# Optimization experiments

Measured on AMD Instinct MI355X. Metric: run time of the kernel, lower is better.

Reference implementation:

```python
import jax, jax.numpy as jnp
import numpy as np

B, T, S, R, D, F = 256, 8, 200, 8, 64, 20


def setup_inputs() -> dict:
    key = jax.random.key(0)
    ks = jax.random.split(key, 8)
    # 0.1 scale keeps attention logits in a reasonable range (like trained embeddings)
    seq = 0.1 * jax.random.normal(ks[0], (B, S, D), dtype=jnp.float32)
    delta_t_n = jax.random.uniform(ks[1], (B, S), dtype=jnp.float32)  # normalized time gaps
    target = 0.1 * jax.random.normal(ks[2], (B, T, D), dtype=jnp.float32)
    target_value = 0.1 * jax.random.normal(ks[3], (B, T, R, D), dtype=jnp.float32)
    valid_mask = jax.random.randint(ks[4], (B, 1, S, 1), 0, 2, dtype=jnp.int32)
    rel_emb = 0.1 * jax.random.normal(ks[5], (R, D), dtype=jnp.float32)
    freq_real = 0.1 * jax.random.normal(ks[6], (R, F), dtype=jnp.float32)
    freq_imag = 0.1 * jax.random.normal(ks[7], (R, F), dtype=jnp.float32)
    return dict(seq=seq, delta_t_n=delta_t_n, target=target, target_value=target_value,
                valid_mask=valid_mask, rel_emb=rel_emb, freq_real=freq_real, freq_imag=freq_imag)


def _idft_decay(delta_t_n, freq_real, freq_imag):
    # freqs: concat(linspace(0,1,F)/2, -linspace(0,1,F)/2) -> [2F]
    f = jnp.linspace(0.0, 1.0, F, dtype=jnp.float32) / 2.0
    freqs = jnp.concatenate([f, -f])
    x_real = jnp.concatenate([freq_real, freq_real], axis=-1)   # [R,2F]
    x_imag = jnp.concatenate([freq_imag, -freq_imag], axis=-1)  # [R,2F]
    w = 2.0 * jnp.pi * freqs * delta_t_n[..., None]             # [B,S,2F]
    # [B,S,1,2F] * [1,1,R,2F] -> mean over 2F -> [B,S,R]
    decay = (jnp.cos(w)[:, :, None, :] * x_real[None, None]
             - jnp.sin(w)[:, :, None, :] * x_imag[None, None]).mean(axis=-1) / 2.0
    return decay


def reference(seq, delta_t_n, target, target_value, valid_mask, rel_emb, freq_real, freq_imag):
    # include_val=True branch
    rv = rel_emb[None, None] + target_value              # [B,T,R,D]
    ri = rv * target[:, :, None, :]                      # [B,T,R,D]
    # scores: contraction over D, no [B,T,S,R,D] materialization
    att = jnp.einsum('bsd,btrd->btsr', seq, ri)          # [B,T,S,R]
    att = att - att.max()
    att = jnp.where(valid_mask == 0, -jnp.inf, att)
    att = jax.nn.softmax(att, axis=-2)                   # softmax over seq (S)
    decay = jnp.clip(_idft_decay(delta_t_n, freq_real, freq_imag), 0.0, 1.0)[:, None]  # [B,1,S,R]
    decay = jnp.where(valid_mask == 0, 0.0, decay)
    att = att * decay
    context = jnp.einsum('bsd,btsr->btrd', seq, att)     # [B,T,R,D]
    return context
```

## Files before the change

kernel.cpp:

```cpp
#include <hip/hip_runtime.h>
#include <math.h>

constexpr int kB = 256, kT = 8, kS = 200, kR = 8, kD = 64, kF = 20;

constexpr float kW1 = 3.14159265358979323846f / 19.0f;

__global__ __launch_bounds__(256) void decay_kernel(
    const float* __restrict__ dt,
    const float* __restrict__ fr,
    const float* __restrict__ fi,
    const int*   __restrict__ vm,
    float* __restrict__ dec)
{
    const int b = blockIdx.x;
    const int tid = threadIdx.x;
    const int r = tid >> 5, j = tid & 31;

    float frr[kF], fir[kF];
    {
        const float4* f4 = (const float4*)(fr + r * kF);
        const float4* g4 = (const float4*)(fi + r * kF);
#pragma unroll
        for (int c = 0; c < 5; ++c) {
            float4 a = f4[c], g = g4[c];
            frr[4 * c + 0] = a.x; frr[4 * c + 1] = a.y;
            frr[4 * c + 2] = a.z; frr[4 * c + 3] = a.w;
            fir[4 * c + 0] = g.x; fir[4 * c + 1] = g.y;
            fir[4 * c + 2] = g.z; fir[4 * c + 3] = g.w;
        }
    }

#pragma unroll
    for (int it = 0; it < 7; ++it) {
        const int s = j + 32 * it;
        if (s < kS) {
            const float tt = dt[b * kS + s];
            const bool valid = vm[b * kS + s] != 0;
            float s1, c1;
            __sincosf(kW1 * tt, &s1, &c1);
            float ck = c1, sk = s1;
            float acc = frr[0] + c1 * frr[1] - s1 * fir[1];
#pragma unroll
            for (int k = 2; k < kF; ++k) {
                float cn = ck * c1 - sk * s1;
                float sn = sk * c1 + ck * s1;
                ck = cn; sk = sn;
                acc += ck * frr[k] - sk * fir[k];
            }
            float v = fminf(fmaxf(acc * (1.0f / (2.0f * kF)), 0.f), 1.f);
            dec[(b * kR + r) * kS + s] = valid ? v : 0.f;
        }
    }
}

__global__ __launch_bounds__(256) void rda_main(
    const float* __restrict__ seq,
    const float* __restrict__ target,
    const float* __restrict__ tv,
    const int*   __restrict__ vm,
    const float* __restrict__ rel,
    const float* __restrict__ dec,
    float* __restrict__ out)
{
    __shared__ float ri[kR * kD];
    __shared__ float att[kR][kS];

    const int o = blockIdx.x;
    const int b = o & 255, t = o >> 8;
    const int bt = b * kT + t;
    const int tid = threadIdx.x, wave = tid >> 6, lane = tid & 63;

    {
        const float* tvb = tv + (size_t)bt * kR * kD;
        const float* tgb = target + (size_t)bt * kD;
        for (int idx = tid; idx < kR * kD; idx += 256)
            ri[idx] = (rel[idx] + tvb[idx]) * tgb[idx & 63];
    }
    __syncthreads();

    if (tid < kS) {
        const int s = tid;
        const bool valid = vm[b * kS + s] != 0;
        const float4* seqrow = (const float4*)(seq + (size_t)(b * kS + s) * kD);
        float a[kR];
#pragma unroll
        for (int r = 0; r < kR; ++r) a[r] = 0.f;
#pragma unroll
        for (int uu = 0; uu < kD / 4; ++uu) {
            float4 sv = seqrow[uu];
#pragma unroll
            for (int r = 0; r < kR; ++r) {
                float4 rv = ((const float4*)(ri + r * kD))[uu];
                a[r] += sv.x * rv.x + sv.y * rv.y + sv.z * rv.z + sv.w * rv.w;
            }
        }
#pragma unroll
        for (int r = 0; r < kR; ++r)
            att[r][s] = valid ? a[r] : -INFINITY;
    }
    __syncthreads();

    float pa[2][4];
#pragma unroll
    for (int h = 0; h < 2; ++h) {
        const int r = 2 * wave + h;
        const float* row = &att[r][0];
        float a0 = row[lane];
        float a1 = row[lane + 64];
        float a2 = row[lane + 128];
        float a3 = (lane < kS - 192) ? row[lane + 192] : -INFINITY;
        float m = fmaxf(fmaxf(a0, a1), fmaxf(a2, a3));
#pragma unroll
        for (int off = 32; off; off >>= 1) m = fmaxf(m, __shfl_xor(m, off));
        float e0 = __expf(a0 - m), e1 = __expf(a1 - m), e2 = __expf(a2 - m);
        float e3 = (lane < kS - 192) ? __expf(a3 - m) : 0.f;
        float ssum = e0 + e1 + e2 + e3;
#pragma unroll
        for (int off = 32; off; off >>= 1) ssum += __shfl_xor(ssum, off);
        const float inv = 1.0f / ssum;
        const float* dg = dec + ((size_t)b * kR + r) * kS;
        pa[h][0] = e0 * inv * dg[lane];
        pa[h][1] = e1 * inv * dg[lane + 64];
        pa[h][2] = e2 * inv * dg[lane + 128];
        pa[h][3] = (lane < kS - 192) ? e3 * inv * dg[lane + 192] : 0.f;
    }

    {
        float acc0 = 0.f, acc1 = 0.f;
        const float* sq = seq + (size_t)b * kS * kD + lane;
#pragma unroll
        for (int s = 0; s < kS; ++s) {
            float sv = sq[(size_t)s * kD];
            float a0 = __int_as_float(
                __builtin_amdgcn_readlane(__float_as_int(pa[0][s >> 6]), s & 63));
            float a1 = __int_as_float(
                __builtin_amdgcn_readlane(__float_as_int(pa[1][s >> 6]), s & 63));
            acc0 += sv * a0;
            acc1 += sv * a1;
        }
        float* ob = out + (size_t)bt * kR * kD;
        ob[(2 * wave + 0) * kD + lane] = acc0;
        ob[(2 * wave + 1) * kD + lane] = acc1;
    }
}

extern "C" void kernel_launch(void* const* d_in, const int* in_sizes, int n_in,
                              void* d_out, int out_size, void* d_ws, size_t ws_size,
                              hipStream_t stream) {
    const float* seq    = (const float*)d_in[0];
    const float* dt     = (const float*)d_in[1];
    const float* target = (const float*)d_in[2];
    const float* tv     = (const float*)d_in[3];
    const int*   vm     = (const int*)  d_in[4];
    const float* rel    = (const float*)d_in[5];
    const float* fr     = (const float*)d_in[6];
    const float* fi     = (const float*)d_in[7];
    float* out = (float*)d_out;
    float* dec = (float*)d_ws;

    decay_kernel<<<kB, 256, 0, stream>>>(dt, fr, fi, vm, dec);
    rda_main<<<kB * kT, 256, 0, stream>>>(seq, target, tv, vm, rel, dec, out);
}
```

Before: 108.3 us.

## Use split-bf16 MFMA for score and context matmuls, two targets per block

```diff
diff --git a/kernel.cpp b/kernel.cpp
--- a/kernel.cpp
+++ b/kernel.cpp
@@ -2,14 +2,26 @@
 #include <math.h>
 
 constexpr int kB = 256, kT = 8, kS = 200, kR = 8, kD = 64, kF = 20;
-
 constexpr float kW1 = 3.14159265358979323846f / 19.0f;
 
+typedef __attribute__((ext_vector_type(8))) short s16x8;
+typedef __attribute__((ext_vector_type(4))) float f32x4;
+
+union F8 { s16x8 v; unsigned short u[8]; };
+
+__device__ __forceinline__ unsigned short bf_hi(float x, float& hf) {
+    unsigned u = __float_as_uint(x) & 0xffff0000u;
+    hf = __uint_as_float(u);
+    return (unsigned short)(u >> 16);
+}
+__device__ __forceinline__ unsigned short bf_rne(float x) {
+    unsigned v = __float_as_uint(x);
+    return (unsigned short)((v + 0x7fffu + ((v >> 16) & 1u)) >> 16);
+}
+
 __global__ __launch_bounds__(256) void decay_kernel(
-    const float* __restrict__ dt,
-    const float* __restrict__ fr,
-    const float* __restrict__ fi,
-    const int*   __restrict__ vm,
+    const float* __restrict__ dt, const float* __restrict__ fr,
+    const float* __restrict__ fi, const int* __restrict__ vm,
     float* __restrict__ dec)
 {
     const int b = blockIdx.x;
@@ -23,13 +35,10 @@
 #pragma unroll
         for (int c = 0; c < 5; ++c) {
             float4 a = f4[c], g = g4[c];
-            frr[4 * c + 0] = a.x; frr[4 * c + 1] = a.y;
-            frr[4 * c + 2] = a.z; frr[4 * c + 3] = a.w;
-            fir[4 * c + 0] = g.x; fir[4 * c + 1] = g.y;
-            fir[4 * c + 2] = g.z; fir[4 * c + 3] = g.w;
-        }
-    }
-
+            frr[4*c+0]=a.x; frr[4*c+1]=a.y; frr[4*c+2]=a.z; frr[4*c+3]=a.w;
+            fir[4*c+0]=g.x; fir[4*c+1]=g.y; fir[4*c+2]=g.z; fir[4*c+3]=g.w;
+        }
+    }
 #pragma unroll
     for (int it = 0; it < 7; ++it) {
         const int s = j + 32 * it;
@@ -53,7 +62,7 @@
     }
 }
 
-__global__ __launch_bounds__(256) void rda_main(
+__global__ __launch_bounds__(256) void rda_mfma(
     const float* __restrict__ seq,
     const float* __restrict__ target,
     const float* __restrict__ tv,
@@ -62,85 +71,125 @@
     const float* __restrict__ dec,
     float* __restrict__ out)
 {
-    __shared__ float ri[kR * kD];
-    __shared__ float att[kR][kS];
-
-    const int o = blockIdx.x;
-    const int b = o & 255, t = o >> 8;
-    const int bt = b * kT + t;
-    const int tid = threadIdx.x, wave = tid >> 6, lane = tid & 63;
-
-    {
-        const float* tvb = tv + (size_t)bt * kR * kD;
-        const float* tgb = target + (size_t)bt * kD;
-        for (int idx = tid; idx < kR * kD; idx += 256)
-            ri[idx] = (rel[idx] + tvb[idx]) * tgb[idx & 63];
+    __shared__ unsigned short riBh[16][72], riBl[16][72];
+    __shared__ float attr[16][212];
+    __shared__ unsigned short ath[16][232], atl[16][232];
+
+    const int o = blockIdx.x, b = o & 255, g = o >> 8, t0 = 2 * g;
+    const int tid = threadIdx.x, w = tid >> 6, l = tid & 63;
+    const int lm = l & 15, lq = l >> 4;
+
+    {
+        const int n = tid >> 4, d0 = (tid & 15) * 4;
+        const int tl = n >> 3, r = n & 7;
+        const int btl = b * kT + t0 + tl;
+        float4 rv  = *(const float4*)(rel + r * kD + d0);
+        float4 tvv = *(const float4*)(tv + ((size_t)btl * kR + r) * kD + d0);
+        float4 tg  = *(const float4*)(target + (size_t)btl * kD + d0);
+        float x[4] = {(rv.x+tvv.x)*tg.x, (rv.y+tvv.y)*tg.y,
+                      (rv.z+tvv.z)*tg.z, (rv.w+tvv.w)*tg.w};
+        ushort4 h, lo; float hf;
+        h.x = bf_hi(x[0], hf); lo.x = bf_rne(x[0] - hf);
+        h.y = bf_hi(x[1], hf); lo.y = bf_rne(x[1] - hf);
+        h.z = bf_hi(x[2], hf); lo.z = bf_rne(x[2] - hf);
+        h.w = bf_hi(x[3], hf); lo.w = bf_rne(x[3] - hf);
+        *(ushort4*)&riBh[n][d0] = h;
+        *(ushort4*)&riBl[n][d0] = lo;
     }
     __syncthreads();
 
-    if (tid < kS) {
-        const int s = tid;
-        const bool valid = vm[b * kS + s] != 0;
-        const float4* seqrow = (const float4*)(seq + (size_t)(b * kS + s) * kD);
-        float a[kR];
-#pragma unroll
-        for (int r = 0; r < kR; ++r) a[r] = 0.f;
-#pragma unroll
-        for (int uu = 0; uu < kD / 4; ++uu) {
-            float4 sv = seqrow[uu];
-#pragma unroll
-            for (int r = 0; r < kR; ++r) {
-                float4 rv = ((const float4*)(ri + r * kD))[uu];
-                a[r] += sv.x * rv.x + sv.y * rv.y + sv.z * rv.z + sv.w * rv.w;
-            }
-        }
-#pragma unroll
-        for (int r = 0; r < kR; ++r)
-            att[r][s] = valid ? a[r] : -INFINITY;
+    for (int Mt = w; Mt < 13; Mt += 4) {
+        const int srow = min(Mt * 16 + lm, kS - 1);
+        const float* sp = seq + ((size_t)b * kS + srow) * kD;
+        F8 ah[2], al[2];
+#pragma unroll
+        for (int Kt = 0; Kt < 2; ++Kt) {
+            const int d0 = Kt * 32 + lq * 8;
+            float4 x0 = *(const float4*)(sp + d0);
+            float4 x1 = *(const float4*)(sp + d0 + 4);
+            float xs[8] = {x0.x,x0.y,x0.z,x0.w,x1.x,x1.y,x1.z,x1.w};
+#pragma unroll
+            for (int i = 0; i < 8; ++i) {
+                float hf; ah[Kt].u[i] = bf_hi(xs[i], hf);
+                al[Kt].u[i] = bf_rne(xs[i] - hf);
+            }
+        }
+        f32x4 acc = {0.f, 0.f, 0.f, 0.f};
+#pragma unroll
+        for (int Kt = 0; Kt < 2; ++Kt) {
+            F8 bh, bl;
+            bh.v = *(const s16x8*)&riBh[lm][Kt * 32 + lq * 8];
+            bl.v = *(const s16x8*)&riBl[lm][Kt * 32 + lq * 8];
+            acc = __builtin_amdgcn_mfma_f32_16x16x32_bf16(ah[Kt].v, bh.v, acc, 0, 0, 0);
+            acc = __builtin_amdgcn_mfma_f32_16x16x32_bf16(ah[Kt].v, bl.v, acc, 0, 0, 0);
+            acc = __builtin_amdgcn_mfma_f32_16x16x32_bf16(al[Kt].v, bh.v, acc, 0, 0, 0);
+        }
+        *(f32x4*)&attr[lm][Mt * 16 + lq * 4] = acc;
     }
     __syncthreads();
 
-    float pa[2][4];
-#pragma unroll
-    for (int h = 0; h < 2; ++h) {
-        const int r = 2 * wave + h;
-        const float* row = &att[r][0];
-        float a0 = row[lane];
-        float a1 = row[lane + 64];
-        float a2 = row[lane + 128];
-        float a3 = (lane < kS - 192) ? row[lane + 192] : -INFINITY;
-        float m = fmaxf(fmaxf(a0, a1), fmaxf(a2, a3));
-#pragma unroll
-        for (int off = 32; off; off >>= 1) m = fmaxf(m, __shfl_xor(m, off));
-        float e0 = __expf(a0 - m), e1 = __expf(a1 - m), e2 = __expf(a2 - m);
-        float e3 = (lane < kS - 192) ? __expf(a3 - m) : 0.f;
-        float ssum = e0 + e1 + e2 + e3;
-#pragma unroll
-        for (int off = 32; off; off >>= 1) ssum += __shfl_xor(ssum, off);
-        const float inv = 1.0f / ssum;
-        const float* dg = dec + ((size_t)b * kR + r) * kS;
-        pa[h][0] = e0 * inv * dg[lane];
-        pa[h][1] = e1 * inv * dg[lane + 64];
-        pa[h][2] = e2 * inv * dg[lane + 128];
-        pa[h][3] = (lane < kS - 192) ? e3 * inv * dg[lane + 192] : 0.f;
-    }
-
-    {
-        float acc0 = 0.f, acc1 = 0.f;
-        const float* sq = seq + (size_t)b * kS * kD + lane;
-#pragma unroll
-        for (int s = 0; s < kS; ++s) {
-            float sv = sq[(size_t)s * kD];
-            float a0 = __int_as_float(
-                __builtin_amdgcn_readlane(__float_as_int(pa[0][s >> 6]), s & 63));
-            float a1 = __int_as_float(
-                __builtin_amdgcn_readlane(__float_as_int(pa[1][s >> 6]), s & 63));
-            acc0 += sv * a0;
-            acc1 += sv * a1;
-        }
-        float* ob = out + (size_t)bt * kR * kD;
-        ob[(2 * wave + 0) * kD + lane] = acc0;
-        ob[(2 * wave + 1) * kD + lane] = acc1;
+    {
+        bool ok0 = vm[b * kS + l] != 0;
+        bool ok1 = vm[b * kS + l + 64] != 0;
+        bool ok2 = vm[b * kS + l + 128] != 0;
+        bool ok3 = (l < 8) && (vm[b * kS + 192 + l] != 0);
+        const int s3 = (l < 8) ? 192 + l : kS - 1;
+#pragma unroll
+        for (int j = 0; j < 4; ++j) {
+            const int n = 4 * w + j, r = n & 7;
+            float a0 = ok0 ? attr[n][l]       : -INFINITY;
+            float a1 = ok1 ? attr[n][l + 64]  : -INFINITY;
+            float a2 = ok2 ? attr[n][l + 128] : -INFINITY;
+            float a3 = ok3 ? attr[n][s3]      : -INFINITY;
+            float m = fmaxf(fmaxf(a0, a1), fmaxf(a2, a3));
+#pragma unroll
+            for (int off = 32; off; off >>= 1) m = fmaxf(m, __shfl_xor(m, off));
+            float e0 = __expf(a0 - m), e1 = __expf(a1 - m);
+            float e2 = __expf(a2 - m), e3 = ok3 ? __expf(a3 - m) : 0.f;
+            float ssum = e0 + e1 + e2 + e3;
+#pragma unroll
+            for (int off = 32; off; off >>= 1) ssum += __shfl_xor(ssum, off);
+            const float inv = 1.0f / ssum;
+            const float* dg = dec + ((size_t)b * kR + r) * kS;
+            float p0 = e0 * inv * dg[l];
+            float p1 = e1 * inv * dg[l + 64];
+            float p2 = e2 * inv * dg[l + 128];
+            float p3 = ok3 ? e3 * inv * dg[192 + l] : 0.f;
+            float hf;
+            ath[n][l]       = bf_hi(p0, hf); atl[n][l]       = bf_rne(p0 - hf);
+            ath[n][l + 64]  = bf_hi(p1, hf); atl[n][l + 64]  = bf_rne(p1 - hf);
+            ath[n][l + 128] = bf_hi(p2, hf); atl[n][l + 128] = bf_rne(p2 - hf);
+            if (l < 32) {
+                float pv = (l < 8) ? p3 : 0.f;
+                ath[n][192 + l] = bf_hi(pv, hf); atl[n][192 + l] = bf_rne(pv - hf);
+            }
+        }
+    }
+    __syncthreads();
+
+    {
+        const int dcol = w * 16 + lm;
+        f32x4 acc = {0.f, 0.f, 0.f, 0.f};
+        for (int Kt = 0; Kt < 7; ++Kt) {
+            F8 bh, bl;
+#pragma unroll
+            for (int i = 0; i < 8; ++i) {
+                const int s = Kt * 32 + lq * 8 + i;
+                float x = (s < kS) ? seq[((size_t)b * kS + s) * kD + dcol] : 0.f;
+                float hf; bh.u[i] = bf_hi(x, hf); bl.u[i] = bf_rne(x - hf);
+            }
+            F8 ahh, alo;
+            ahh.v = *(const s16x8*)&ath[lm][Kt * 32 + lq * 8];
+            alo.v = *(const s16x8*)&atl[lm][Kt * 32 + lq * 8];
+            acc = __builtin_amdgcn_mfma_f32_16x16x32_bf16(ahh.v, bh.v, acc, 0, 0, 0);
+            acc = __builtin_amdgcn_mfma_f32_16x16x32_bf16(ahh.v, bl.v, acc, 0, 0, 0);
+            acc = __builtin_amdgcn_mfma_f32_16x16x32_bf16(alo.v, bh.v, acc, 0, 0, 0);
+        }
+#pragma unroll
+        for (int i = 0; i < 4; ++i) {
+            const int n = lq * 4 + i, tl = n >> 3, r = n & 7;
+            out[(((size_t)(b * kT + t0 + tl)) * kR + r) * kD + dcol] = acc[i];
+        }
     }
 }
 
@@ -159,5 +208,5 @@
     float* dec = (float*)d_ws;
 
     decay_kernel<<<kB, 256, 0, stream>>>(dt, fr, fi, vm, dec);
-    rda_main<<<kB * kT, 256, 0, stream>>>(seq, target, tv, vm, rel, dec, out);
-}
+    rda_mfma<<<kB * 4, 256, 0, stream>>>(seq, target, tv, vm, rel, dec, out);
+}
```

New measurement: 92.37 us. -14.7%, faster.
